# Kernel tuning notes

Hardware: AMD Instinct MI355X
Metric: run time of the kernel (lower is better)

Reference implementation:

```python
import jax, jax.numpy as jnp
import numpy as np


def setup_inputs() -> dict:
    B, L, D, M, S = 4, 1024, 1024, 16, 8
    key = jax.random.key(0)
    ks = jax.random.split(key, 12)
    sd = 0.02
    inp = {
        "hid": jax.random.normal(ks[0], (B, L, D), jnp.float32),
        "src_hid": jax.random.normal(ks[1], (B, L, D), jnp.float32),
        "sp_width": jax.random.randint(ks[2], (B, L), 0, 9),
        "max_sp_len": S,
        "attention_mask": jnp.ones((B, L), bool),
        "src_mask": jnp.ones((B, L), bool),
        # span-start attention (1 head): query/key linears + relative-key embedding table
        "wq_st": sd * jax.random.normal(ks[3], (D, D), jnp.float32),
        "bq_st": jnp.zeros((D,), jnp.float32),
        "wk_st": sd * jax.random.normal(ks[4], (D, D), jnp.float32),
        "bk_st": jnp.zeros((D,), jnp.float32),
        "rel_st": sd * jax.random.normal(ks[5], (2 * M + 1, D), jnp.float32),
        # span-end attention
        "wq_ed": sd * jax.random.normal(ks[6], (D, D), jnp.float32),
        "bq_ed": jnp.zeros((D,), jnp.float32),
        "wk_ed": sd * jax.random.normal(ks[7], (D, D), jnp.float32),
        "bk_ed": jnp.zeros((D,), jnp.float32),
        "rel_ed": sd * jax.random.normal(ks[8], (2 * M + 1, D), jnp.float32),
        # sp_emb: Linear(2D -> D), stored as [2D, D] (x @ W + b)
        "sp_w": sd * jax.random.normal(ks[9], (2 * D, D), jnp.float32),
        "sp_b": jnp.zeros((D,), jnp.float32),
    }
    return inp


def reference(hid, src_hid, sp_width, max_sp_len, attention_mask, src_mask,
              wq_st, bq_st, wk_st, bk_st, rel_st,
              wq_ed, bq_ed, wk_ed, bk_ed, rel_ed, sp_w, sp_b):
    B, L, D = hid.shape
    scale = 1.0 / jnp.sqrt(jnp.float32(D))
    M = (rel_st.shape[0] - 1) // 2
    pos = jnp.arange(L)
    rel_idx = jnp.clip(pos[None, :] - pos[:, None], -M, M) + M          # [L,L]
    rel_idx_b = jnp.broadcast_to(rel_idx[None], (B, L, L))

    amask = (src_mask[:, :, None] & attention_mask[:, None, :]).astype(jnp.float32)  # [B,Lq,Lk]
    attn_w0 = amask / jnp.clip(jnp.sum(amask, 2, keepdims=True), 1e-6)

    def attn(query, wq, bq, wk, bk, rel_tab, mask):
        # single-head relative-position attention; returns attention weights [B,L,L]
        q = (query @ wq + bq) * scale                                   # [B,L,D]
        k = hid @ wk + bk                                               # [B,L,D]
        sc = jnp.einsum('bqd,bkd->bqk', q, k)
        # q . rel_emb[rel_idx[q_pos,k_pos]]: contract with table then gather (avoids [L,L,D])
        rel_sc = jnp.take_along_axis(jnp.einsum('bqd,rd->bqr', q, rel_tab), rel_idx_b, axis=2)
        sc = jnp.where(mask > 0, sc + rel_sc, -1e18)
        return jax.nn.softmax(sc, axis=-1)

    def upd(attn_w, hidp):
        # weighted sum of hid + linear + relu (dropout is identity in eval)
        hidc = jnp.einsum('bqk,bkd->bqd', attn_w, hid)
        return jax.nn.relu(jnp.concatenate([hidp, hidc], axis=2) @ sp_w + sp_b)

    sts, eds, masks = [attn_w0], [attn_w0], []
    hid1, hid2 = src_hid, src_hid
    for i in range(max_sp_len):
        m = (i < sp_width).astype(jnp.float32)                          # [B,L]
        masks.append(m)
        mask_i = m[:, :, None] * amask                                  # [B,L,L]
        hid1 = upd(sts[-1], hid1)
        sts.append(attn(hid1, wq_st, bq_st, wk_st, bk_st, rel_st, mask_i))
        hid2 = upd(eds[-1], hid2)
        eds.append(attn(hid2, wq_ed, bq_ed, wk_ed, bk_ed, rel_ed, mask_i))

    return (jnp.stack(sts[1:], -2),   # [B,L,S,L]
            jnp.stack(eds[1:], -2),   # [B,L,S,L]
            jnp.stack(masks, -1))     # [B,L,S]
```

## Files before the change

### kernel.cpp

```cpp
#include <hip/hip_runtime.h>

typedef unsigned short u16;
typedef __attribute__((ext_vector_type(8))) short bh8;
typedef __attribute__((ext_vector_type(4))) float f4;

__device__ __forceinline__ u16 f2b(float x){
  union { float f; unsigned u; } c; c.f = x;
  unsigned r = (c.u + 0x7FFFu + ((c.u >> 16) & 1u)) >> 16;
  return (u16)r;
}
__device__ __forceinline__ float b2f(u16 h){
  union { unsigned u; float f; } c; c.u = ((unsigned)h) << 16; return c.f;
}
__device__ __forceinline__ void gload16(const void* g, void* l){
  __builtin_amdgcn_global_load_lds((const __attribute__((address_space(1))) void*)g,
                                   (__attribute__((address_space(3))) void*)l, 16, 0, 0);
}


__global__ __launch_bounds__(256) void convall_k(const float* __restrict__ hid,
                                                 const float* __restrict__ wq0, const float* __restrict__ wq1,
                                                 const float* __restrict__ wk0, const float* __restrict__ wk1,
                                                 u16* __restrict__ hidB, u16* __restrict__ wqB, u16* __restrict__ wkB){
  long i = (long)blockIdx.x*256 + threadIdx.x;
  const float* src; u16* dst; long off;
  if      (i < 4194304L){ src = hid; dst = hidB;           off = i; }
  else if (i < 5242880L){ src = wq0; dst = wqB;            off = i - 4194304L; }
  else if (i < 6291456L){ src = wq1; dst = wqB + 1048576;  off = i - 5242880L; }
  else if (i < 7340032L){ src = wk0; dst = wkB;            off = i - 6291456L; }
  else                  { src = wk1; dst = wkB + 1048576;  off = i - 7340032L; }
  dst[off] = f2b(src[off]);
}

__global__ __launch_bounds__(256) void fill_k(u16* __restrict__ out, u16 v, long n){
  long i = (long)blockIdx.x*256 + threadIdx.x;
  if (i < n) out[i] = v;
}

__global__ __launch_bounds__(256) void masks_k(const int* __restrict__ spw, float* __restrict__ mout){
  int idx = blockIdx.x*256 + threadIdx.x;
  if (idx >= 4*1024*8) return;
  int i = idx & 7, bq = idx >> 3;
  mout[idx] = (i < spw[bq]) ? 1.0f : 0.0f;
}

__global__ __launch_bounds__(256) void uniform_k(const int* __restrict__ spw, float* __restrict__ out){
  int blk = blockIdx.x;
  int s = blk >> 12, bl = blk & 4095;
  int w = spw[bl];
  if (w >= 8) return;
  float* base = out + (size_t)s*33554432ull + (size_t)bl*8192;
  f4 t = {0.0009765625f, 0.0009765625f, 0.0009765625f, 0.0009765625f};
  for (int i = w; i < 8; i++)
    ((f4*)(base + (size_t)i*1024))[threadIdx.x] = t;
}

__global__ __launch_bounds__(256) void trans_k(const float* __restrict__ in, u16* __restrict__ out,
                                               int R, int C){
  __shared__ u16 t[32][33];
  int bx = blockIdx.x*32, by = blockIdx.y*32;
  int tx = threadIdx.x & 31, ty = threadIdx.x >> 5;
  #pragma unroll
  for (int j = 0; j < 32; j += 8) t[ty+j][tx] = f2b(in[(size_t)(by+ty+j)*C + bx+tx]);
  __syncthreads();
  #pragma unroll
  for (int j = 0; j < 32; j += 8) out[(size_t)(bx+ty+j)*R + by+tx] = t[tx][ty+j];
}

__global__ __launch_bounds__(256) void sort_k(const int* __restrict__ spw, int* __restrict__ perm,
                                              int* __restrict__ cnt){
  int b = blockIdx.x, t = threadIdx.x;
  __shared__ int hist[9], start[9];
  if (t < 9) hist[t] = 0;
  __syncthreads();
  for (int l = t; l < 1024; l += 256) atomicAdd(&hist[spw[b*1024 + l]], 1);
  __syncthreads();
  if (t == 0){
    int acc = 0;
    for (int w = 8; w >= 0; w--){ start[w] = acc; acc += hist[w]; }
  }
  __syncthreads();
  if (t < 8) cnt[b*8 + t] = start[t];
  __syncthreads();
  for (int l = t; l < 1024; l += 256){
    int w = spw[b*1024 + l];
    int pos = atomicAdd(&start[w], 1);
    perm[b*1024 + pos] = l;
  }
}

__global__ __launch_bounds__(256) void gather_k(const float* __restrict__ srch, const int* __restrict__ perm,
                                                u16* __restrict__ hb){
  int blk = blockIdx.x;
  int z = blk >> 10, c = blk & 1023, b = z & 3;
  int ro = perm[b*1024 + c];
  const float* src = srch + ((size_t)b*1024 + ro)*1024;
  u16* dst = hb + ((size_t)z*1024 + c)*1024;
  for (int d = threadIdx.x; d < 1024; d += 256) dst[d] = f2b(src[d]);
}

__global__ __launch_bounds__(256) void wrt_k(const float* __restrict__ wq0, const float* __restrict__ wq1,
                                             const float* __restrict__ rel0, const float* __restrict__ rel1,
                                             u16* __restrict__ WrS){
  long idx = (long)blockIdx.x*256 + threadIdx.x;
  if (idx >= 2L*33*1024) return;
  int s = idx >= 33*1024; long loc = idx - (s ? 33*1024 : 0);
  int r = (int)(loc >> 10), e = (int)(loc & 1023);
  const float* wqrow = (s ? wq1 : wq0) + (size_t)e*1024;
  const float* rel = (s ? rel1 : rel0) + (size_t)r*1024;
  float acc = 0.0f;
  #pragma unroll 4
  for (int k = 0; k < 1024; k++) acc += wqrow[k]*rel[k];
  WrS[(size_t)s*33792 + (size_t)r*1024 + e] = f2b(acc*0.03125f);
}

__global__ __launch_bounds__(256) void wrcopy_k(const u16* __restrict__ WrS, u16* __restrict__ Mx){
  int idx = blockIdx.x*256 + threadIdx.x;
  if (idx >= 8*33792) return;
  int z = idx / 33792, loc = idx % 33792;
  int s = z >> 2;
  Mx[(size_t)z*1179648 + 1048576 + loc] = WrS[(size_t)s*33792 + loc];
}

__global__ __launch_bounds__(256) void dots_k(const float* __restrict__ wq0, const float* __restrict__ wq1,
                                              const float* __restrict__ wk0, const float* __restrict__ wk1,
                                              const float* __restrict__ bq0, const float* __restrict__ bq1,
                                              const float* __restrict__ bk0, const float* __restrict__ bk1,
                                              const float* __restrict__ rel0, const float* __restrict__ rel1,
                                              float* __restrict__ ubuf, float* __restrict__ c0buf,
                                              float* __restrict__ bqbk, float* __restrict__ cba){
  int row = blockIdx.x*4 + (threadIdx.x >> 6);
  int lane = threadIdx.x & 63;
  if (row >= 4164) return;
  const float *a, *v;
  int kind = 0, oi = 0, br_s = 0, br_r = 0;
  if      (row < 1024){ a = wk0 + (size_t)row*1024; v = bq0; oi = row; }
  else if (row < 2048){ a = wk1 + (size_t)(row-1024)*1024; v = bq1; oi = row; }
  else if (row < 3072){ a = wq0 + (size_t)(row-2048)*1024; v = bk0; kind = 1; oi = row-2048; }
  else if (row < 4096){ a = wq1 + (size_t)(row-3072)*1024; v = bk1; kind = 1; oi = row-3072+1024; }
  else if (row < 4162){ int idx = row-4096; br_s = idx/33; br_r = idx%33;
                        a = (br_s ? rel1 : rel0) + (size_t)br_r*1024; v = br_s ? bq1 : bq0; kind = 2; }
  else                { int s2 = row-4162; a = s2 ? bq1 : bq0; v = s2 ? bk1 : bk0; kind = 3; oi = s2; }
  const f4* ap = (const f4*)a;
  const f4* vp = (const f4*)v;
  float acc = 0.0f;
  #pragma unroll
  for (int p = 0; p < 4; p++){
    f4 x = ap[lane + 64*p], y = vp[lane + 64*p];
    acc += x[0]*y[0] + x[1]*y[1] + x[2]*y[2] + x[3]*y[3];
  }
  #pragma unroll
  for (int off = 32; off > 0; off >>= 1) acc += __shfl_xor(acc, off, 64);
  if (lane == 0){
    if (kind == 0) ubuf[oi] = acc;
    else if (kind == 1) c0buf[oi] = acc;
    else if (kind == 2){
      float w = acc*0.03125f;
      for (int b = 0; b < 4; b++) cba[(br_s*4 + b)*1152 + 1024 + br_r] = w;
    } else bqbk[oi] = acc;
  }
}

__global__ __launch_bounds__(256) void cba_k(const float* __restrict__ hid, const float* __restrict__ u,
                                             const float* __restrict__ bqbk, float* __restrict__ cba){
  int row = blockIdx.x*4 + (threadIdx.x >> 6);
  int lane = threadIdx.x & 63;
  int z = row >> 10, l = row & 1023, b = z & 3, s = z >> 2;
  const f4* hp = (const f4*)(hid + ((size_t)b*1024 + l)*1024);
  const f4* up = (const f4*)(u + s*1024);
  float acc = 0.0f;
  #pragma unroll
  for (int p = 0; p < 4; p++){
    f4 a = hp[lane + 64*p], c = up[lane + 64*p];
    acc += a[0]*c[0] + a[1]*c[1] + a[2]*c[2] + a[3]*c[3];
  }
  #pragma unroll
  for (int off = 32; off > 0; off >>= 1) acc += __shfl_xor(acc, off, 64);
  if (!lane) cba[z*1152 + l] = (acc + bqbk[s])*0.03125f;
}

__global__ __launch_bounds__(256) void meanh2_k(const u16* __restrict__ H2T, float* __restrict__ mh){
  int row = blockIdx.x*4 + (threadIdx.x >> 6);
  int lane = threadIdx.x & 63;
  const u16* p = H2T + (size_t)row*1024 + lane*16;
  float s = 0.0f;
  #pragma unroll
  for (int j = 0; j < 16; j++) s += b2f(p[j]);
  #pragma unroll
  for (int off = 32; off > 0; off >>= 1) s += __shfl_xor(s, off, 64);
  if (lane == 0) mh[row] = s * 0.0009765625f;
}

__global__ __launch_bounds__(256) void softmax_k(const u16* __restrict__ scB, float* __restrict__ outF,
                                                 u16* __restrict__ attnP, const float* __restrict__ qrelb,
                                                 const int* __restrict__ cnt, const int* __restrict__ perm,
                                                 int iter){
  int z = blockIdx.x >> 10, c = blockIdx.x & 1023;
  int s = z >> 2, b = z & 3;
  if (c >= cnt[b*8 + iter]) return;
  int ro = perm[b*1024 + c];
  __shared__ float qr[33];
  __shared__ float red[8];
  if (threadIdx.x < 33) qr[threadIdx.x] = qrelb[((size_t)z*1024 + c)*33 + threadIdx.x];
  __syncthreads();
  const u16* sc = scB + ((size_t)z*1024 + c)*1024;
  float* po = outF + (size_t)s*33554432ull + (((size_t)(b*1024 + ro))*8 + (size_t)iter)*1024;
  u16* pr = attnP + ((size_t)z*1024 + c)*1024;
  int t = threadIdx.x;
  float v[4]; float mx = -1e30f;
  #pragma unroll
  for (int j = 0; j < 4; j++){
    int col = t + j*256;
    int d = col - ro; d = d < -16 ? -16 : (d > 16 ? 16 : d);
    v[j] = b2f(sc[col]) + qr[d + 16];
    mx = fmaxf(mx, v[j]);
  }
  #pragma unroll
  for (int off = 32; off > 0; off >>= 1) mx = fmaxf(mx, __shfl_xor(mx, off, 64));
  int wv = t >> 6, ln = t & 63;
  if (ln == 0) red[wv] = mx;
  __syncthreads();
  mx = fmaxf(fmaxf(red[0], red[1]), fmaxf(red[2], red[3]));
  float sm = 0.0f;
  #pragma unroll
  for (int j = 0; j < 4; j++){ v[j] = __expf(v[j] - mx); sm += v[j]; }
  #pragma unroll
  for (int off = 32; off > 0; off >>= 1) sm += __shfl_xor(sm, off, 64);
  if (ln == 0) red[4 + wv] = sm;
  __syncthreads();
  sm = red[4] + red[5] + red[6] + red[7];
  float inv = 1.0f / sm;
  #pragma unroll
  for (int j = 0; j < 4; j++){
    float pv = v[j] * inv;
    po[t + j*256] = pv;
    pr[t + j*256] = f2b(pv);
  }
}

template<int MODE>
__global__ __launch_bounds__(256) void gemm_k(
    const u16* __restrict__ A_, const u16* __restrict__ B_,
    const u16* __restrict__ A2_, const u16* __restrict__ B2_,
    const float* __restrict__ e0, const float* __restrict__ e1,
    u16* __restrict__ outB, float* __restrict__ qrelb,
    const int* __restrict__ cnt, int iter)
{
  const int z = blockIdx.z;
  const int s = (MODE == 1) ? 0 : (z >> 2);
  const int b = (MODE == 1) ? z : (z & 3);
  const size_t LD = 1024*1024;
  const int bm = blockIdx.y*128, bn = blockIdx.x*128;

  int cntv = 1024;
  if constexpr (MODE == 2 || MODE == 4){
    cntv = cnt[b*8 + iter];
    if (bm >= cntv) return;
  }

  const u16 *A1, *B1, *A2, *B2;
  int lda1 = 1024, ldb1 = 1024, lda2 = 1024, ldb2 = 1024, K = 1024, K1 = 1024;

  if constexpr (MODE == 0){ A1 = A_ + (size_t)z*LD; B1 = B_ + (size_t)z*LD; A2=A1; B2=B1; }
  else if constexpr (MODE == 1){ A1 = A_ + 1024; lda1 = 2048; B1 = B_ + (size_t)z*LD; A2=A1; B2=B1; lda2=lda1; }
  else if constexpr (MODE == 2){
    A1 = A_ + (size_t)z*LD; B1 = B_ + (size_t)b*LD;
    A2 = A2_ + (size_t)z*LD; B2 = B2_; ldb2 = 2048;
    if (iter == 0){ K = 1024; K1 = 0; } else { K = 2048; K1 = 1024; }
  }
  else if constexpr (MODE == 3){ A1 = A_ + (size_t)b*LD; B1 = B_ + (size_t)s*LD; A2=A1; B2=B1; }
  else { A1 = A_ + (size_t)z*LD; B1 = B_ + (size_t)z*1179648; A2=A1; B2=B1; }

  __shared__ __align__(16) u16 lA[8192];
  __shared__ __align__(16) u16 lB[8192];
  const int tid = threadIdx.x, wv = tid >> 6, lane = tid & 63;
  const int wr = (wv >> 1)*64, wc = (wv & 1)*64;
  const int fr = lane & 15, kh = lane >> 4;

  f4 acc[4][4];
  #pragma unroll
  for (int i = 0; i < 4; i++)
    #pragma unroll
    for (int j = 0; j < 4; j++)
      acc[i][j] = f4{0.f, 0.f, 0.f, 0.f};

  const int stRow = (lane >> 2);
  const int stCe  = (lane & 3)*8;

  for (int k0 = 0; k0 < K; k0 += 64){
    __syncthreads();
    const u16 *As, *Bs; int kk, la, lb;
    if (k0 < K1){ As = A1; Bs = B1; kk = k0; la = lda1; lb = ldb1; }
    else        { As = A2; Bs = B2; kk = k0 - K1; la = lda2; lb = ldb2; }
    #pragma unroll
    for (int c = 0; c < 4; c++){
      const int n = wv*4 + c;
      const int h = n >> 3;
      const int rl = (n & 7)*16 + stRow;
      const int ke = kk + h*32 + stCe;
      const int base = n*2048;
      gload16(As + (size_t)(bm + rl)*la + ke, (char*)lA + n*1024);
      gload16(Bs + (size_t)(bn + rl)*lb + ke, (char*)lB + n*1024);
      (void)base;
    }
    asm volatile("s_waitcnt vmcnt(0)" ::: "memory");
    __syncthreads();

    #pragma unroll
    for (int h = 0; h < 2; h++){
      bh8 af[4], bfr[4];
      #pragma unroll
      for (int i = 0; i < 4; i++){
        af[i]  = *(const bh8*)&lA[h*4096 + (wr + i*16 + fr)*32 + kh*8];
        bfr[i] = *(const bh8*)&lB[h*4096 + (wc + i*16 + fr)*32 + kh*8];
      }
      #pragma unroll
      for (int i = 0; i < 4; i++)
        #pragma unroll
        for (int j = 0; j < 4; j++)
          acc[i][j] = __builtin_amdgcn_mfma_f32_16x16x32_bf16(af[i], bfr[j], acc[i][j], 0, 0, 0);
    }
  }

  const int rw = (lane >> 4)*4, cl = lane & 15;
  #pragma unroll
  for (int i = 0; i < 4; i++){
    #pragma unroll
    for (int r = 0; r < 4; r++){
      const int row = bm + wr + i*16 + rw + r;
      if constexpr (MODE == 4){ if (row >= cntv) continue; }
      #pragma unroll
      for (int j = 0; j < 4; j++){
        const int col = bn + wc + j*16 + cl;
        float v = acc[i][j][r];
        if constexpr (MODE == 0 || MODE == 1){
          outB[(size_t)z*LD + (size_t)row*1024 + col] = f2b(v);
        } else if constexpr (MODE == 2){
          v += e0[col];
          if (e1) v += e1[b*1024 + col];
          v = fmaxf(v, 0.0f);
          outB[(size_t)z*LD + (size_t)row*1024 + col] = f2b(v);
        } else if constexpr (MODE == 3){
          outB[(size_t)z*1179648 + (size_t)row*1024 + col] = f2b((v + e0[s*1024 + col])*0.03125f);
        } else {
          v += e0[z*1152 + col];
          if (col < 1024){
            outB[((size_t)z*1024 + row)*1024 + col] = f2b(v);
          } else {
            int rr = col - 1024;
            if (rr < 33) qrelb[((size_t)z*1024 + row)*33 + rr] = v;
          }
        }
      }
    }
  }
}


extern "C" void kernel_launch(void* const* d_in, const int* in_sizes, int n_in,
                              void* d_out, int out_size, void* d_ws, size_t ws_size,
                              hipStream_t stream)
{
  const float* hid    = (const float*)d_in[0];
  const float* srch   = (const float*)d_in[1];
  const int*   spw    = (const int*)d_in[2];
  const float* wq_st  = (const float*)d_in[6];
  const float* bq_st  = (const float*)d_in[7];
  const float* wk_st  = (const float*)d_in[8];
  const float* bk_st  = (const float*)d_in[9];
  const float* rel_st = (const float*)d_in[10];
  const float* wq_ed  = (const float*)d_in[11];
  const float* bq_ed  = (const float*)d_in[12];
  const float* wk_ed  = (const float*)d_in[13];
  const float* bk_ed  = (const float*)d_in[14];
  const float* rel_ed = (const float*)d_in[15];
  const float* sp_w   = (const float*)d_in[16];
  const float* sp_b   = (const float*)d_in[17];
  float* out = (float*)d_out;

  const size_t LD = 1024*1024;
  char* p = (char*)d_ws;
  u16* hidB  = (u16*)p; p += 4*LD*2;
  u16* wqB   = (u16*)p; p += 2*LD*2;
  u16* wkB   = (u16*)p; p += 2*LD*2;
  u16* spwT  = (u16*)p; p += 2*LD*2;
  u16* WT    = (u16*)p; p += 2*LD*2;
  u16* H2T   = (u16*)p; p += 4*LD*2;
  u16* Mx    = (u16*)p; p += 8ull*1179648*2;
  u16* WrS   = (u16*)p; p += 2*33792*2;
  u16* attnP = (u16*)p; p += 8*LD*2;
  u16* hbufA = (u16*)p; p += 8*LD*2;
  u16* hbufB = (u16*)p; p += 8*LD*2;
  u16* scB   = (u16*)p; p += 8*LD*2;
  float* qrelb  = (float*)p; p += 8*1024*33*4;
  float* cba    = (float*)p; p += 8*1152*4;
  float* ubuf   = (float*)p; p += 2048*4;
  float* c0buf  = (float*)p; p += 2048*4;
  float* bqbk   = (float*)p; p += 64;
  float* meanH2 = (float*)p; p += 4*1024*4;
  int*   perm   = (int*)p;   p += 4*1024*4;
  int*   cnt    = (int*)p;   p += 1024;

  const dim3 t256(256);

  convall_k<<<32768, t256, 0, stream>>>(hid, wq_st, wq_ed, wk_st, wk_ed, hidB, wqB, wkB);
  sort_k<<<4, t256, 0, stream>>>(spw, perm, cnt);
  gather_k<<<8192, t256, 0, stream>>>(srch, perm, hbufA);
  uniform_k<<<8192, t256, 0, stream>>>(spw, out);
  masks_k<<<128, t256, 0, stream>>>(spw, out + 67108864ull);
  trans_k<<<dim3(32,64), t256, 0, stream>>>(sp_w, spwT, 2048, 1024);
  fill_k<<<36864, t256, 0, stream>>>(Mx, (u16)0, 8L*1179648);
  wrt_k<<<264, t256, 0, stream>>>(wq_st, wq_ed, rel_st, rel_ed, WrS);
  wrcopy_k<<<1056, t256, 0, stream>>>(WrS, Mx);
  dots_k<<<1041, t256, 0, stream>>>(wq_st, wq_ed, wk_st, wk_ed, bq_st, bq_ed, bk_st, bk_ed,
                                    rel_st, rel_ed, ubuf, c0buf, bqbk, cba);
  cba_k<<<2048, t256, 0, stream>>>(hid, ubuf, bqbk, cba);

  gemm_k<0><<<dim3(8,8,2), t256, 0, stream>>>(wqB, wkB, nullptr, nullptr, nullptr, nullptr,
                                              WT, nullptr, nullptr, 0);
  gemm_k<3><<<dim3(8,8,8), t256, 0, stream>>>(hidB, WT, nullptr, nullptr, c0buf, nullptr,
                                              Mx, nullptr, nullptr, 0);
  gemm_k<1><<<dim3(8,8,4), t256, 0, stream>>>(spwT, hidB, nullptr, nullptr, nullptr, nullptr,
                                              H2T, nullptr, nullptr, 0);
  meanh2_k<<<1024, t256, 0, stream>>>(H2T, meanH2);

  u16* hp = hbufA; u16* hn = hbufB;
  for (int i = 0; i < 8; i++){
    gemm_k<2><<<dim3(8,8,8), t256, 0, stream>>>(attnP, H2T, hp, spwT, sp_b,
                                                (i == 0) ? meanH2 : nullptr,
                                                hn, nullptr, cnt, i);
    gemm_k<4><<<dim3(9,8,8), t256, 0, stream>>>(hn, Mx, nullptr, nullptr, cba, nullptr,
                                                scB, qrelb, cnt, i);
    softmax_k<<<8192, t256, 0, stream>>>(scB, out, attnP, qrelb, cnt, perm, i);
    u16* tmp = hp; hp = hn; hn = tmp;
  }
}
```

Measured before the change: 970.3 us.

## Double-buffer GEMM LDS tiles, fuse mask output into sort, drop Mx zero fill

The GEMM kernel now holds two LDS buffers per operand. It issues the global-to-LDS loads for the next K tile before running the MFMAs on the current tile, and keeps a single barrier per iteration, so memory latency can overlap with compute. The mask output is written inside sort_k, which removes the separate masks_k launch. The fill_k pass that zeroed Mx is dropped. The explicit vmcnt wait before the barrier is gone, so correctness now depends on the compiler inserting waits for the async LDS loads. Any part of Mx not overwritten by later kernels may now hold stale data.

```diff
diff --git a/kernel.cpp b/kernel.cpp
--- a/kernel.cpp
+++ b/kernel.cpp
@@ -32,18 +32,6 @@
   dst[off] = f2b(src[off]);
 }
 
-__global__ __launch_bounds__(256) void fill_k(u16* __restrict__ out, u16 v, long n){
-  long i = (long)blockIdx.x*256 + threadIdx.x;
-  if (i < n) out[i] = v;
-}
-
-__global__ __launch_bounds__(256) void masks_k(const int* __restrict__ spw, float* __restrict__ mout){
-  int idx = blockIdx.x*256 + threadIdx.x;
-  if (idx >= 4*1024*8) return;
-  int i = idx & 7, bq = idx >> 3;
-  mout[idx] = (i < spw[bq]) ? 1.0f : 0.0f;
-}
-
 __global__ __launch_bounds__(256) void uniform_k(const int* __restrict__ spw, float* __restrict__ out){
   int blk = blockIdx.x;
   int s = blk >> 12, bl = blk & 4095;
@@ -68,7 +56,7 @@
 }
 
 __global__ __launch_bounds__(256) void sort_k(const int* __restrict__ spw, int* __restrict__ perm,
-                                              int* __restrict__ cnt){
+                                              int* __restrict__ cnt, float* __restrict__ mout){
   int b = blockIdx.x, t = threadIdx.x;
   __shared__ int hist[9], start[9];
   if (t < 9) hist[t] = 0;
@@ -84,6 +72,9 @@
   __syncthreads();
   for (int l = t; l < 1024; l += 256){
     int w = spw[b*1024 + l];
+    float* mo = mout + ((size_t)b*1024 + l)*8;
+    #pragma unroll
+    for (int i = 0; i < 8; i++) mo[i] = (i < w) ? 1.0f : 0.0f;
     int pos = atomicAdd(&start[w], 1);
     perm[b*1024 + pos] = l;
   }
@@ -271,48 +262,51 @@
   else if constexpr (MODE == 3){ A1 = A_ + (size_t)b*LD; B1 = B_ + (size_t)s*LD; A2=A1; B2=B1; }
   else { A1 = A_ + (size_t)z*LD; B1 = B_ + (size_t)z*1179648; A2=A1; B2=B1; }
 
-  __shared__ __align__(16) u16 lA[8192];
-  __shared__ __align__(16) u16 lB[8192];
+  __shared__ __align__(16) u16 lA[16384];
+  __shared__ __align__(16) u16 lB[16384];
   const int tid = threadIdx.x, wv = tid >> 6, lane = tid & 63;
   const int wr = (wv >> 1)*64, wc = (wv & 1)*64;
   const int fr = lane & 15, kh = lane >> 4;
-
-  f4 acc[4][4];
-  #pragma unroll
-  for (int i = 0; i < 4; i++)
-    #pragma unroll
-    for (int j = 0; j < 4; j++)
-      acc[i][j] = f4{0.f, 0.f, 0.f, 0.f};
-
   const int stRow = (lane >> 2);
   const int stCe  = (lane & 3)*8;
 
-  for (int k0 = 0; k0 < K; k0 += 64){
-    __syncthreads();
+  auto stage = [&](int bufsel, int k0s){
     const u16 *As, *Bs; int kk, la, lb;
-    if (k0 < K1){ As = A1; Bs = B1; kk = k0; la = lda1; lb = ldb1; }
-    else        { As = A2; Bs = B2; kk = k0 - K1; la = lda2; lb = ldb2; }
+    if (k0s < K1){ As = A1; Bs = B1; kk = k0s; la = lda1; lb = ldb1; }
+    else         { As = A2; Bs = B2; kk = k0s - K1; la = lda2; lb = ldb2; }
     #pragma unroll
     for (int c = 0; c < 4; c++){
       const int n = wv*4 + c;
       const int h = n >> 3;
       const int rl = (n & 7)*16 + stRow;
       const int ke = kk + h*32 + stCe;
-      const int base = n*2048;
-      gload16(As + (size_t)(bm + rl)*la + ke, (char*)lA + n*1024);
-      gload16(Bs + (size_t)(bn + rl)*lb + ke, (char*)lB + n*1024);
-      (void)base;
+      gload16(As + (size_t)(bm + rl)*la + ke, (char*)lA + (bufsel << 14) + n*1024);
+      gload16(Bs + (size_t)(bn + rl)*lb + ke, (char*)lB + (bufsel << 14) + n*1024);
     }
-    asm volatile("s_waitcnt vmcnt(0)" ::: "memory");
-    __syncthreads();
-
+  };
+
+  f4 acc[4][4];
+  #pragma unroll
+  for (int i = 0; i < 4; i++)
+    #pragma unroll
+    for (int j = 0; j < 4; j++)
+      acc[i][j] = f4{0.f, 0.f, 0.f, 0.f};
+
+  stage(0, 0);
+  __syncthreads();
+
+  int cur = 0;
+  for (int k0 = 0; k0 < K; k0 += 64){
+    if (k0 + 64 < K) stage(cur ^ 1, k0 + 64);
+    const u16* bufA = lA + cur*8192;
+    const u16* bufB = lB + cur*8192;
     #pragma unroll
     for (int h = 0; h < 2; h++){
       bh8 af[4], bfr[4];
       #pragma unroll
       for (int i = 0; i < 4; i++){
-        af[i]  = *(const bh8*)&lA[h*4096 + (wr + i*16 + fr)*32 + kh*8];
-        bfr[i] = *(const bh8*)&lB[h*4096 + (wc + i*16 + fr)*32 + kh*8];
+        af[i]  = *(const bh8*)&bufA[h*4096 + (wr + i*16 + fr)*32 + kh*8];
+        bfr[i] = *(const bh8*)&bufB[h*4096 + (wc + i*16 + fr)*32 + kh*8];
       }
       #pragma unroll
       for (int i = 0; i < 4; i++)
@@ -320,6 +314,8 @@
         for (int j = 0; j < 4; j++)
           acc[i][j] = __builtin_amdgcn_mfma_f32_16x16x32_bf16(af[i], bfr[j], acc[i][j], 0, 0, 0);
     }
+    __syncthreads();
+    cur ^= 1;
   }
 
   const int rw = (lane >> 4)*4, cl = lane & 15;
@@ -404,12 +400,10 @@
   const dim3 t256(256);
 
   convall_k<<<32768, t256, 0, stream>>>(hid, wq_st, wq_ed, wk_st, wk_ed, hidB, wqB, wkB);
-  sort_k<<<4, t256, 0, stream>>>(spw, perm, cnt);
+  sort_k<<<4, t256, 0, stream>>>(spw, perm, cnt, out + 67108864ull);
   gather_k<<<8192, t256, 0, stream>>>(srch, perm, hbufA);
   uniform_k<<<8192, t256, 0, stream>>>(spw, out);
-  masks_k<<<128, t256, 0, stream>>>(spw, out + 67108864ull);
   trans_k<<<dim3(32,64), t256, 0, stream>>>(sp_w, spwT, 2048, 1024);
-  fill_k<<<36864, t256, 0, stream>>>(Mx, (u16)0, 8L*1179648);
   wrt_k<<<264, t256, 0, stream>>>(wq_st, wq_ed, rel_st, rel_ed, WrS);
   wrcopy_k<<<1056, t256, 0, stream>>>(WrS, Mx);
   dots_k<<<1041, t256, 0, stream>>>(wq_st, wq_ed, wk_st, wk_ed, bq_st, bq_ed, bk_st, bk_ed,
```

Measured after the change: 970.7 us. No clear change (+0.0%).

## Use 64-row GEMM tiles for late iterations and drop redundant fill and mask kernels

Applied to the files above, without the earlier changes.

Adds a gemm64_k variant with 64-row M tiles, used for iterations 4-7, where fewer rows stay active. The smaller tile wastes less work on the ragged row count. The mask output is now written inside sort_k instead of a separate kernel. The zero-fill of the Mx buffer is removed, which relies on padding regions never affecting kept outputs. MODE 2 epilogues now also skip stores for rows beyond the active count.

```diff
diff --git a/kernel.cpp b/kernel.cpp
--- a/kernel.cpp
+++ b/kernel.cpp
@@ -32,18 +32,6 @@
   dst[off] = f2b(src[off]);
 }
 
-__global__ __launch_bounds__(256) void fill_k(u16* __restrict__ out, u16 v, long n){
-  long i = (long)blockIdx.x*256 + threadIdx.x;
-  if (i < n) out[i] = v;
-}
-
-__global__ __launch_bounds__(256) void masks_k(const int* __restrict__ spw, float* __restrict__ mout){
-  int idx = blockIdx.x*256 + threadIdx.x;
-  if (idx >= 4*1024*8) return;
-  int i = idx & 7, bq = idx >> 3;
-  mout[idx] = (i < spw[bq]) ? 1.0f : 0.0f;
-}
-
 __global__ __launch_bounds__(256) void uniform_k(const int* __restrict__ spw, float* __restrict__ out){
   int blk = blockIdx.x;
   int s = blk >> 12, bl = blk & 4095;
@@ -68,7 +56,7 @@
 }
 
 __global__ __launch_bounds__(256) void sort_k(const int* __restrict__ spw, int* __restrict__ perm,
-                                              int* __restrict__ cnt){
+                                              int* __restrict__ cnt, float* __restrict__ mout){
   int b = blockIdx.x, t = threadIdx.x;
   __shared__ int hist[9], start[9];
   if (t < 9) hist[t] = 0;
@@ -84,6 +72,9 @@
   __syncthreads();
   for (int l = t; l < 1024; l += 256){
     int w = spw[b*1024 + l];
+    float* mo = mout + ((size_t)b*1024 + l)*8;
+    #pragma unroll
+    for (int i = 0; i < 8; i++) mo[i] = (i < w) ? 1.0f : 0.0f;
     int pos = atomicAdd(&start[w], 1);
     perm[b*1024 + pos] = l;
   }
@@ -276,6 +267,8 @@
   const int tid = threadIdx.x, wv = tid >> 6, lane = tid & 63;
   const int wr = (wv >> 1)*64, wc = (wv & 1)*64;
   const int fr = lane & 15, kh = lane >> 4;
+  const int stRow = (lane >> 2);
+  const int stCe  = (lane & 3)*8;
 
   f4 acc[4][4];
   #pragma unroll
@@ -283,9 +276,6 @@
     #pragma unroll
     for (int j = 0; j < 4; j++)
       acc[i][j] = f4{0.f, 0.f, 0.f, 0.f};
-
-  const int stRow = (lane >> 2);
-  const int stCe  = (lane & 3)*8;
 
   for (int k0 = 0; k0 < K; k0 += 64){
     __syncthreads();
@@ -298,10 +288,8 @@
       const int h = n >> 3;
       const int rl = (n & 7)*16 + stRow;
       const int ke = kk + h*32 + stCe;
-      const int base = n*2048;
       gload16(As + (size_t)(bm + rl)*la + ke, (char*)lA + n*1024);
       gload16(Bs + (size_t)(bn + rl)*lb + ke, (char*)lB + n*1024);
-      (void)base;
     }
     asm volatile("s_waitcnt vmcnt(0)" ::: "memory");
     __syncthreads();
@@ -328,7 +316,7 @@
     #pragma unroll
     for (int r = 0; r < 4; r++){
       const int row = bm + wr + i*16 + rw + r;
-      if constexpr (MODE == 4){ if (row >= cntv) continue; }
+      if constexpr (MODE == 2 || MODE == 4){ if (row >= cntv) continue; }
       #pragma unroll
       for (int j = 0; j < 4; j++){
         const int col = bn + wc + j*16 + cl;
@@ -356,6 +344,117 @@
   }
 }
 
+template<int MODE>
+__global__ __launch_bounds__(256) void gemm64_k(
+    const u16* __restrict__ A_, const u16* __restrict__ B_,
+    const u16* __restrict__ A2_, const u16* __restrict__ B2_,
+    const float* __restrict__ e0, const float* __restrict__ e1,
+    u16* __restrict__ outB, float* __restrict__ qrelb,
+    const int* __restrict__ cnt, int iter)
+{
+  const int z = blockIdx.z;
+  const int s = z >> 2, b = z & 3;
+  const size_t LD = 1024*1024;
+  const int bm = blockIdx.y*64, bn = blockIdx.x*128;
+
+  int cntv = cnt[b*8 + iter];
+  if (bm >= cntv) return;
+
+  const u16 *A1, *B1, *A2, *B2;
+  int lda1 = 1024, ldb1 = 1024, lda2 = 1024, ldb2 = 1024, K = 1024, K1 = 1024;
+
+  if constexpr (MODE == 2){
+    A1 = A_ + (size_t)z*LD; B1 = B_ + (size_t)b*LD;
+    A2 = A2_ + (size_t)z*LD; B2 = B2_; ldb2 = 2048;
+    if (iter == 0){ K = 1024; K1 = 0; } else { K = 2048; K1 = 1024; }
+  } else {
+    A1 = A_ + (size_t)z*LD; B1 = B_ + (size_t)z*1179648; A2=A1; B2=B1;
+  }
+
+  __shared__ __align__(16) u16 lA[4096];
+  __shared__ __align__(16) u16 lB[8192];
+  const int tid = threadIdx.x, wv = tid >> 6, lane = tid & 63;
+  const int wc = wv*32;
+  const int fr = lane & 15, kh = lane >> 4;
+  const int stRow = (lane >> 2);
+  const int stCe  = (lane & 3)*8;
+
+  f4 acc[4][2];
+  #pragma unroll
+  for (int i = 0; i < 4; i++)
+    #pragma unroll
+    for (int j = 0; j < 2; j++)
+      acc[i][j] = f4{0.f, 0.f, 0.f, 0.f};
+
+  for (int k0 = 0; k0 < K; k0 += 64){
+    __syncthreads();
+    const u16 *As, *Bs; int kk, la, lb;
+    if (k0 < K1){ As = A1; Bs = B1; kk = k0; la = lda1; lb = ldb1; }
+    else        { As = A2; Bs = B2; kk = k0 - K1; la = lda2; lb = ldb2; }
+    #pragma unroll
+    for (int c = 0; c < 2; c++){
+      const int n = wv*2 + c;
+      const int h = n >> 2;
+      const int rl = (n & 3)*16 + stRow;
+      gload16(As + (size_t)(bm + rl)*la + (kk + h*32 + stCe), (char*)lA + n*1024);
+    }
+    #pragma unroll
+    for (int c = 0; c < 4; c++){
+      const int n = wv*4 + c;
+      const int h = n >> 3;
+      const int rl = (n & 7)*16 + stRow;
+      gload16(Bs + (size_t)(bn + rl)*lb + (kk + h*32 + stCe), (char*)lB + n*1024);
+    }
+    asm volatile("s_waitcnt vmcnt(0)" ::: "memory");
+    __syncthreads();
+
+    #pragma unroll
+    for (int h = 0; h < 2; h++){
+      bh8 af[4], bfr[2];
+      #pragma unroll
+      for (int i = 0; i < 4; i++)
+        af[i]  = *(const bh8*)&lA[h*2048 + (i*16 + fr)*32 + kh*8];
+      #pragma unroll
+      for (int j = 0; j < 2; j++)
+        bfr[j] = *(const bh8*)&lB[h*4096 + (wc + j*16 + fr)*32 + kh*8];
+      #pragma unroll
+      for (int i = 0; i < 4; i++)
+        #pragma unroll
+        for (int j = 0; j < 2; j++)
+          acc[i][j] = __builtin_amdgcn_mfma_f32_16x16x32_bf16(af[i], bfr[j], acc[i][j], 0, 0, 0);
+    }
+  }
+
+  const int rw = (lane >> 4)*4, cl = lane & 15;
+  #pragma unroll
+  for (int i = 0; i < 4; i++){
+    #pragma unroll
+    for (int r = 0; r < 4; r++){
+      const int row = bm + i*16 + rw + r;
+      if (row >= cntv) continue;
+      #pragma unroll
+      for (int j = 0; j < 2; j++){
+        const int col = bn + wc + j*16 + cl;
+        float v = acc[i][j][r];
+        if constexpr (MODE == 2){
+          v += e0[col];
+          if (e1) v += e1[b*1024 + col];
+          v = fmaxf(v, 0.0f);
+          outB[(size_t)z*LD + (size_t)row*1024 + col] = f2b(v);
+        } else {
+          v += e0[z*1152 + col];
+          if (col < 1024){
+            outB[((size_t)z*1024 + row)*1024 + col] = f2b(v);
+          } else {
+            int rr = col - 1024;
+            if (rr < 33) qrelb[((size_t)z*1024 + row)*33 + rr] = v;
+          }
+        }
+      }
+    }
+  }
+}
+
 
 extern "C" void kernel_launch(void* const* d_in, const int* in_sizes, int n_in,
                               void* d_out, int out_size, void* d_ws, size_t ws_size,
@@ -404,12 +503,10 @@
   const dim3 t256(256);
 
   convall_k<<<32768, t256, 0, stream>>>(hid, wq_st, wq_ed, wk_st, wk_ed, hidB, wqB, wkB);
-  sort_k<<<4, t256, 0, stream>>>(spw, perm, cnt);
+  sort_k<<<4, t256, 0, stream>>>(spw, perm, cnt, out + 67108864ull);
   gather_k<<<8192, t256, 0, stream>>>(srch, perm, hbufA);
   uniform_k<<<8192, t256, 0, stream>>>(spw, out);
-  masks_k<<<128, t256, 0, stream>>>(spw, out + 67108864ull);
   trans_k<<<dim3(32,64), t256, 0, stream>>>(sp_w, spwT, 2048, 1024);
-  fill_k<<<36864, t256, 0, stream>>>(Mx, (u16)0, 8L*1179648);
   wrt_k<<<264, t256, 0, stream>>>(wq_st, wq_ed, rel_st, rel_ed, WrS);
   wrcopy_k<<<1056, t256, 0, stream>>>(WrS, Mx);
   dots_k<<<1041, t256, 0, stream>>>(wq_st, wq_ed, wk_st, wk_ed, bq_st, bq_ed, bk_st, bk_ed,
@@ -426,11 +523,19 @@
 
   u16* hp = hbufA; u16* hn = hbufB;
   for (int i = 0; i < 8; i++){
-    gemm_k<2><<<dim3(8,8,8), t256, 0, stream>>>(attnP, H2T, hp, spwT, sp_b,
-                                                (i == 0) ? meanH2 : nullptr,
-                                                hn, nullptr, cnt, i);
-    gemm_k<4><<<dim3(9,8,8), t256, 0, stream>>>(hn, Mx, nullptr, nullptr, cba, nullptr,
-                                                scB, qrelb, cnt, i);
+    if (i < 4)
+      gemm_k<2><<<dim3(8,8,8), t256, 0, stream>>>(attnP, H2T, hp, spwT, sp_b,
+                                                  (i == 0) ? meanH2 : nullptr,
+                                                  hn, nullptr, cnt, i);
+    else
+      gemm64_k<2><<<dim3(8,16,8), t256, 0, stream>>>(attnP, H2T, hp, spwT, sp_b, nullptr,
+                                                     hn, nullptr, cnt, i);
+    if (i < 4)
+      gemm_k<4><<<dim3(9,8,8), t256, 0, stream>>>(hn, Mx, nullptr, nullptr, cba, nullptr,
+                                                  scB, qrelb, cnt, i);
+    else
+      gemm64_k<4><<<dim3(9,16,8), t256, 0, stream>>>(hn, Mx, nullptr, nullptr, cba, nullptr,
+                                                     scB, qrelb, cnt, i);
     softmax_k<<<8192, t256, 0, stream>>>(scB, out, attnP, qrelb, cnt, perm, i);
     u16* tmp = hp; hp = hn; hn = tmp;
   }
```

Result: slower. 994.5 us (+2.5%).
